# Optimization experiments

Hardware: AMD Instinct MI355X
Metric: run time of the kernel (lower is better)

Reference implementation:

```python
import jax, jax.numpy as jnp
import numpy as np

WIN = 2
PC = 48
IMG = 128
D = PC * WIN * WIN      # token dim == state dim N == 192
NS = IMG // WIN          # 64
L = NS * NS              # 4096 tokens
BATCH = 2


def setup_inputs() -> dict:
    key = jax.random.key(0)
    ks = jax.random.split(key, 8)
    s = 1.0 / np.sqrt(D)  # nn.Linear default init scale
    x = jax.random.normal(ks[0], (BATCH, PC, IMG, IMG), jnp.float32)
    A_log = jnp.log(jax.random.uniform(ks[1], (D, D), jnp.float32, 1.0, 16.0))
    D_param = jnp.ones((D,), jnp.float32)
    W_B = jax.random.uniform(ks[2], (D, D), jnp.float32, -s, s)
    b_B = jax.random.uniform(ks[3], (D,), jnp.float32, -s, s)
    W_C = jax.random.uniform(ks[4], (D, D), jnp.float32, -s, s)
    b_C = jax.random.uniform(ks[5], (D,), jnp.float32, -s, s)
    W_dt = jax.random.uniform(ks[6], (D, D), jnp.float32, -s, s)
    b_dt = jax.random.uniform(ks[7], (D,), jnp.float32, -s, s)
    return {"x": x, "A_log": A_log, "D_param": D_param, "W_B": W_B, "b_B": b_B,
            "W_C": W_C, "b_C": b_C, "W_dt": W_dt, "b_dt": b_dt}


def _forward(x, A_log, D_param, W_B, b_B, W_C, b_C, W_dt, b_dt):
    Bb, C, H, W = x.shape
    w = WIN
    # unfold into non-overlapping windows -> tokens (B, L, D) with D = C*w*w (channel-major)
    t = x.reshape(Bb, C, H // w, w, W // w, w).transpose(0, 1, 2, 4, 3, 5)
    tokens = t.reshape(Bb, C, -1, w * w).transpose(0, 2, 1, 3).reshape(Bb, -1, D)
    Bm = tokens @ W_B.T + b_B                      # (B, L, D) -> state input proj
    Cm = tokens @ W_C.T + b_C                      # (B, L, D) -> state output proj
    dt = jax.nn.softplus(tokens @ W_dt.T + b_dt)   # module applies softplus once
    # selective_scan_fn applies delta = softplus(delta + delta_bias) again (delta_softplus=True)
    delta = jax.nn.softplus(dt + b_dt)             # (B, L, D)
    A = -jnp.exp(A_log)                            # (D, N) with N == D
    u = tokens                                     # (B, L, D)

    def step(h, inp):
        d_l, u_l, B_l, C_l = inp                   # (B,D) (B,D) (B,N) (B,N)
        dA = jnp.exp(d_l[:, :, None] * A[None])    # (B, D, N)
        h = dA * h + (d_l * u_l)[:, :, None] * B_l[:, None, :]
        y = jnp.einsum('bdn,bn->bd', h, C_l)
        return h, y

    h0 = jnp.zeros((Bb, D, D), x.dtype)
    xs = (delta.transpose(1, 0, 2), u.transpose(1, 0, 2),
          Bm.transpose(1, 0, 2), Cm.transpose(1, 0, 2))
    _, ys = jax.lax.scan(step, h0, xs)             # (L, B, D)
    y = ys.transpose(1, 2, 0)                      # (B, D, L)
    y = y + D_param[None, :, None] * u.transpose(0, 2, 1)
    z = jnp.ones_like(y)                           # z = ones in the module
    y = y * (z * jax.nn.sigmoid(z))                # silu(z) gating
    out = y.reshape(Bb, NS, NS, PC, w, w).transpose(0, 3, 1, 4, 2, 5)
    return out.reshape(Bb, PC, NS * w, NS * w)


def reference(x, A_log, D_param, W_B, b_B, W_C, b_C, W_dt, b_dt):
    return _forward(x, A_log, D_param, W_B, b_B, W_C, b_C, W_dt, b_dt)
```

## Files before the change

kernel.cpp:

```cpp
#include <hip/hip_runtime.h>
#include <hip/hip_bf16.h>
#include <math.h>

#define BB   2
#define PCH  48
#define DD   192
#define NSB  64
#define LL   4096
#define NCH  128
#define LCH  32
#define WUP  12
#define NG   8
#define NCK  24
#define SILU1 0.7310585786300049f

typedef float v2f __attribute__((ext_vector_type(2)));
typedef float v4f __attribute__((ext_vector_type(4)));
typedef __bf16 bf16x8 __attribute__((ext_vector_type(8)));
typedef float f32x4 __attribute__((ext_vector_type(4)));

#if __has_builtin(__builtin_amdgcn_exp2f)
#define EXP2(x) __builtin_amdgcn_exp2f(x)
#else
#define EXP2(x) exp2f(x)
#endif

#if __has_builtin(__builtin_elementwise_fma)
static __device__ __forceinline__ v2f fma2(v2f a, v2f b, v2f c) {
    return __builtin_elementwise_fma(a, b, c);
}
#else
static __device__ __forceinline__ v2f fma2(v2f a, v2f b, v2f c) {
    v2f r; r.x = __builtin_fmaf(a.x, b.x, c.x); r.y = __builtin_fmaf(a.y, b.y, c.y);
    return r;
}
#endif

static __device__ __forceinline__ float softplus_(float x) {
    return fmaxf(x, 0.0f) + log1pf(__expf(-fabsf(x)));
}

static __device__ __forceinline__ unsigned short f2bf(float f) {
    unsigned int u = __builtin_bit_cast(unsigned int, f);
    u += 0x7fffu + ((u >> 16) & 1u);
    return (unsigned short)(u >> 16);
}

__global__ void k_tok(const float* __restrict__ x, float* __restrict__ tokens,
                      float* __restrict__ u_t,
                      const float* __restrict__ A_log, float* __restrict__ A2t,
                      const float* __restrict__ W_B, const float* __restrict__ W_C,
                      const float* __restrict__ W_dt,
                      unsigned short* __restrict__ tok_bf,
                      unsigned short* __restrict__ W_bf) {
    __shared__ float lds[64 * 196];
    int b  = blockIdx.x >> 6;
    int hb = blockIdx.x & 63;
    int tid = threadIdx.x;
    for (int t = blockIdx.x * 256 + tid; t < DD * DD; t += 128 * 256) {
        int n = t / DD, d = t - n * DD;
        A2t[t] = -__expf(A_log[d * DD + n]) * 1.4426950408889634f;
    }
    for (int t = blockIdx.x * 256 + tid; t < 3 * DD * DD; t += 128 * 256) {
        int mat = t / (DD * DD), r = t - mat * DD * DD;
        const float* W = (mat == 0) ? W_B : (mat == 1 ? W_C : W_dt);
        W_bf[t] = f2bf(W[r]);
    }
    for (int idx = tid; idx < 48 * 2 * 128; idx += 256) {
        int c = idx >> 8; int r = idx & 255; int i = r >> 7; int w = r & 127;
        float v = x[((b * 48 + c) * 128 + (hb * 2 + i)) * 128 + w];
        int wb = w >> 1, j = w & 1;
        lds[wb * 196 + c * 4 + i * 2 + j] = v;
    }
    __syncthreads();
    for (int idx = tid; idx < 64 * 192; idx += 256) {
        int wb = idx / 192, d = idx - wb * 192;
        float v = lds[wb * 196 + d];
        size_t o = (size_t)(b * 4096 + hb * 64 + wb) * 192 + d;
        tokens[o] = v;
        tok_bf[o] = f2bf(v);
    }
    for (int idx = tid; idx < 64 * 192; idx += 256) {
        int d = idx >> 6, wb = idx & 63;
        u_t[(size_t)(b * 192 + d) * 4096 + hb * 64 + wb] = lds[wb * 196 + d];
    }
}

__global__ __launch_bounds__(256) void k_proj(
        const unsigned short* __restrict__ tok_bf,
        const unsigned short* __restrict__ W_bf,
        const float* __restrict__ b_B, const float* __restrict__ b_C,
        const float* __restrict__ b_dt,
        float* __restrict__ Bm, float* __restrict__ Cm,
        float* __restrict__ delta) {
    int tid  = threadIdx.x;
    int lane = tid & 63;
    int wv   = tid >> 6;
    int m0   = blockIdx.x * 16;
    int mat  = blockIdx.y;
    int lrow = lane & 15;
    int koff = (lane >> 4) * 8;

    const unsigned short* ap = tok_bf + (size_t)(m0 + lrow) * 192 + koff;
    bf16x8 a[6];
    #pragma unroll
    for (int k0 = 0; k0 < 6; ++k0)
        a[k0] = *reinterpret_cast<const bf16x8*>(ap + k0 * 32);

    f32x4 acc[3];
    #pragma unroll
    for (int jt = 0; jt < 3; ++jt) {
        #pragma unroll
        for (int r = 0; r < 4; ++r) acc[jt][r] = 0.f;
    }
    #pragma unroll
    for (int jt = 0; jt < 3; ++jt) {
        int j = wv * 48 + jt * 16 + lrow;
        const unsigned short* bp = W_bf + (size_t)(mat * 192 + j) * 192 + koff;
        #pragma unroll
        for (int k0 = 0; k0 < 6; ++k0) {
            bf16x8 bv = *reinterpret_cast<const bf16x8*>(bp + k0 * 32);
            acc[jt] = __builtin_amdgcn_mfma_f32_16x16x32_bf16(a[k0], bv, acc[jt],
                                                              0, 0, 0);
        }
    }

    int col = lane & 15;
    int rb  = (lane >> 4) * 4;
    #pragma unroll
    for (int jt = 0; jt < 3; ++jt) {
        int j = wv * 48 + jt * 16 + col;
        #pragma unroll
        for (int r = 0; r < 4; ++r) {
            int m = m0 + rb + r;
            float z = acc[jt][r];
            size_t o = (size_t)m * 192 + j;
            if (mat == 0)       Bm[o] = z + b_B[j];
            else if (mat == 1)  Cm[o] = z + b_C[j];
            else {
                float bd = b_dt[j];
                delta[o] = softplus_(softplus_(z + bd) + bd);
            }
        }
    }
}

__global__ __launch_bounds__(512, 6) void k_scan(
        const float* __restrict__ delta, const float* __restrict__ tokens,
        const float* __restrict__ Bm, const float* __restrict__ Cm,
        const float* __restrict__ A2t, float* __restrict__ y_t) {
    __shared__ float ytile[LCH * 65];
    int tid = threadIdx.x;
    for (int i = tid; i < LCH * 65; i += 512) ytile[i] = 0.0f;
    __syncthreads();

    int lane = tid & 63;
    int ng   = tid >> 6;
    int blk  = blockIdx.x;
    int c    = blk & (NCH - 1);
    int rest = blk >> 7;
    int dg   = rest % 3, b = rest / 3;
    int d    = dg * 64 + lane;
    int n0   = ng * NCK;

    v2f A2[NCK / 2], h[NCK / 2];
    #pragma unroll
    for (int p = 0; p < NCK / 2; ++p) {
        A2[p].x = A2t[(n0 + 2 * p) * 192 + d];
        A2[p].y = A2t[(n0 + 2 * p + 1) * 192 + d];
        h[p].x = 0.f; h[p].y = 0.f;
    }

    int l0     = c * LCH;
    int nwarm  = (c == 0) ? 0 : WUP;
    int base   = (b * 4096 + l0 - nwarm) * 192;
    int ubase  = __builtin_amdgcn_readfirstlane(base + n0);
    const float* bp = Bm + ubase;
    const float* cp = Cm + ubase;
    const float* dp = delta + base + d;
    const float* up = tokens + base + d;

    float dlt = dp[0], uv = up[0];
    int s = 0;
    #pragma unroll 4
    for (int t = 0; t < nwarm; ++t, ++s) {
        float dn = dp[(s + 1) * 192], un = up[(s + 1) * 192];
        const v4f* B4 = (const v4f*)(bp + s * 192);
        v4f bq[NCK / 4];
        #pragma unroll
        for (int q = 0; q < NCK / 4; ++q) bq[q] = B4[q];
        float du = dlt * uv;
        v2f dlt2; dlt2.x = dlt; dlt2.y = dlt;
        v2f du2;  du2.x = du;   du2.y = du;
        #pragma unroll
        for (int q = 0; q < NCK / 4; ++q) {
            v2f blo = __builtin_shufflevector(bq[q], bq[q], 0, 1);
            v2f bhi = __builtin_shufflevector(bq[q], bq[q], 2, 3);
            v2f e0 = dlt2 * A2[2 * q];
            v2f e1 = dlt2 * A2[2 * q + 1];
            v2f dA0; dA0.x = EXP2(e0.x); dA0.y = EXP2(e0.y);
            v2f dA1; dA1.x = EXP2(e1.x); dA1.y = EXP2(e1.y);
            h[2 * q]     = fma2(dA0, h[2 * q],     du2 * blo);
            h[2 * q + 1] = fma2(dA1, h[2 * q + 1], du2 * bhi);
        }
        dlt = dn; uv = un;
    }
    #pragma unroll 4
    for (int t = 0; t < LCH; ++t, ++s) {
        float dn = dp[(s + 1) * 192], un = up[(s + 1) * 192];
        const v4f* B4 = (const v4f*)(bp + s * 192);
        const v4f* C4 = (const v4f*)(cp + s * 192);
        v4f bq[NCK / 4], cq[NCK / 4];
        #pragma unroll
        for (int q = 0; q < NCK / 4; ++q) { bq[q] = B4[q]; cq[q] = C4[q]; }
        float du = dlt * uv;
        v2f dlt2; dlt2.x = dlt; dlt2.y = dlt;
        v2f du2;  du2.x = du;   du2.y = du;
        v2f acc2; acc2.x = 0.f; acc2.y = 0.f;
        #pragma unroll
        for (int q = 0; q < NCK / 4; ++q) {
            v2f blo = __builtin_shufflevector(bq[q], bq[q], 0, 1);
            v2f bhi = __builtin_shufflevector(bq[q], bq[q], 2, 3);
            v2f clo = __builtin_shufflevector(cq[q], cq[q], 0, 1);
            v2f chi = __builtin_shufflevector(cq[q], cq[q], 2, 3);
            v2f e0 = dlt2 * A2[2 * q];
            v2f e1 = dlt2 * A2[2 * q + 1];
            v2f dA0; dA0.x = EXP2(e0.x); dA0.y = EXP2(e0.y);
            v2f dA1; dA1.x = EXP2(e1.x); dA1.y = EXP2(e1.y);
            h[2 * q]     = fma2(dA0, h[2 * q],     du2 * blo);
            h[2 * q + 1] = fma2(dA1, h[2 * q + 1], du2 * bhi);
            acc2 = fma2(h[2 * q],     clo, acc2);
            acc2 = fma2(h[2 * q + 1], chi, acc2);
        }
        atomicAdd(&ytile[t * 65 + lane], acc2.x + acc2.y);
        dlt = dn; uv = un;
    }
    __syncthreads();
    for (int idx = tid; idx < LCH * 64; idx += 512) {
        int dd = idx >> 5, t = idx & (LCH - 1);
        y_t[((size_t)(b * 192 + dg * 64 + dd)) * 4096 + l0 + t] =
            ytile[t * 65 + dd];
    }
}

__global__ void k_fin(const float* __restrict__ y_t, const float* __restrict__ u_t,
                      const float* __restrict__ Dp, float* __restrict__ out) {
    __shared__ float v[3 * 4224];
    int b  = blockIdx.x >> 6;
    int a1 = blockIdx.x & 63;
    int d0 = 3 * a1;
    int tid = threadIdx.x;
    for (int idx = tid; idx < 3 * 4096; idx += 256) {
        int e = idx >> 12, l = idx & 4095;
        size_t o = ((size_t)(b * 192 + d0 + e)) * 4096 + l;
        float val = (y_t[o] + Dp[d0 + e] * u_t[o]) * SILU1;
        v[e * 4224 + l + (l >> 5)] = val;
    }
    __syncthreads();
    for (int o = tid; o < 12288; o += 256) {
        int cc = o >> 8;
        int i  = (o >> 7) & 1;
        int w  = o & 127;
        int a2 = w >> 1, j = w & 1;
        int r  = a2 * 192 + cc * 4 + i * 2 + j;
        int e  = r >> 12, l = r & 4095;
        out[((size_t)((b * 48 + cc) * 128 + (a1 * 2 + i))) * 128 + w] =
            v[e * 4224 + l + (l >> 5)];
    }
}

extern "C" void kernel_launch(void* const* d_in, const int* in_sizes, int n_in,
                              void* d_out, int out_size, void* d_ws, size_t ws_size,
                              hipStream_t stream) {
    const float* x     = (const float*)d_in[0];
    const float* A_log = (const float*)d_in[1];
    const float* Dp    = (const float*)d_in[2];
    const float* W_B   = (const float*)d_in[3];
    const float* b_B   = (const float*)d_in[4];
    const float* W_C   = (const float*)d_in[5];
    const float* b_C   = (const float*)d_in[6];
    const float* W_dt  = (const float*)d_in[7];
    const float* b_dt  = (const float*)d_in[8];
    float* out = (float*)d_out;

    const size_t TOK = (size_t)BB * LL * DD;
    float* ws = (float*)d_ws;
    float* tokens = ws;
    float* u_t    = tokens + TOK;
    float* Bm     = u_t + TOK;
    float* Cm     = Bm + TOK;
    float* delta  = Cm + TOK;
    float* A2t    = delta + TOK;
    float* y_t    = A2t + (size_t)DD * DD;
    unsigned short* tok_bf = (unsigned short*)(y_t + TOK);
    unsigned short* W_bf   = tok_bf + TOK;

    k_tok<<<dim3(BB * NSB), dim3(256), 0, stream>>>(x, tokens, u_t, A_log, A2t,
                                                    W_B, W_C, W_dt, tok_bf, W_bf);
    k_proj<<<dim3(512, 3), dim3(256), 0, stream>>>(tok_bf, W_bf, b_B, b_C, b_dt,
                                                   Bm, Cm, delta);
    k_scan<<<dim3(BB * 3 * NCH), dim3(512), 0, stream>>>(delta, tokens, Bm, Cm,
                                                         A2t, y_t);
    k_fin<<<dim3(BB * NSB), dim3(256), 0, stream>>>(y_t, u_t, Dp, out);
}
```

Before: 129.6 us.

## Fuse finalize epilogue into scan kernel and drop u_t/y_t intermediates

The scan kernel now caches each chunk's u values in shared memory, applies the D skip term and the constant SiLU gate, and writes straight into the output image layout. This removes the k_fin launch, the transposed u_t store in k_tok, and the y_t round-trip through global memory. In exchange the output stores from the scan epilogue are scattered with integer div/mod index math and are poorly coalesced, and the scan uses a little more shared memory.

```diff
diff --git a/kernel.cpp b/kernel.cpp
--- a/kernel.cpp
+++ b/kernel.cpp
@@ -47,7 +47,6 @@
 }
 
 __global__ void k_tok(const float* __restrict__ x, float* __restrict__ tokens,
-                      float* __restrict__ u_t,
                       const float* __restrict__ A_log, float* __restrict__ A2t,
                       const float* __restrict__ W_B, const float* __restrict__ W_C,
                       const float* __restrict__ W_dt,
@@ -79,10 +78,6 @@
         size_t o = (size_t)(b * 4096 + hb * 64 + wb) * 192 + d;
         tokens[o] = v;
         tok_bf[o] = f2bf(v);
-    }
-    for (int idx = tid; idx < 64 * 192; idx += 256) {
-        int d = idx >> 6, wb = idx & 63;
-        u_t[(size_t)(b * 192 + d) * 4096 + hb * 64 + wb] = lds[wb * 196 + d];
     }
 }
 
@@ -148,8 +143,10 @@
 __global__ __launch_bounds__(512, 6) void k_scan(
         const float* __restrict__ delta, const float* __restrict__ tokens,
         const float* __restrict__ Bm, const float* __restrict__ Cm,
-        const float* __restrict__ A2t, float* __restrict__ y_t) {
+        const float* __restrict__ A2t, const float* __restrict__ Dp,
+        float* __restrict__ out) {
     __shared__ float ytile[LCH * 65];
+    __shared__ float utile[LCH * 65];
     int tid = threadIdx.x;
     for (int i = tid; i < LCH * 65; i += 512) ytile[i] = 0.0f;
     __syncthreads();
@@ -208,6 +205,7 @@
     #pragma unroll 4
     for (int t = 0; t < LCH; ++t, ++s) {
         float dn = dp[(s + 1) * 192], un = up[(s + 1) * 192];
+        if (ng == 0) utile[t * 65 + lane] = uv;
         const v4f* B4 = (const v4f*)(bp + s * 192);
         const v4f* C4 = (const v4f*)(cp + s * 192);
         v4f bq[NCK / 4], cq[NCK / 4];
@@ -236,36 +234,20 @@
         dlt = dn; uv = un;
     }
     __syncthreads();
+
+    #pragma unroll 1
     for (int idx = tid; idx < LCH * 64; idx += 512) {
         int dd = idx >> 5, t = idx & (LCH - 1);
-        y_t[((size_t)(b * 192 + dg * 64 + dd)) * 4096 + l0 + t] =
-            ytile[t * 65 + dd];
-    }
-}
-
-__global__ void k_fin(const float* __restrict__ y_t, const float* __restrict__ u_t,
-                      const float* __restrict__ Dp, float* __restrict__ out) {
-    __shared__ float v[3 * 4224];
-    int b  = blockIdx.x >> 6;
-    int a1 = blockIdx.x & 63;
-    int d0 = 3 * a1;
-    int tid = threadIdx.x;
-    for (int idx = tid; idx < 3 * 4096; idx += 256) {
-        int e = idx >> 12, l = idx & 4095;
-        size_t o = ((size_t)(b * 192 + d0 + e)) * 4096 + l;
-        float val = (y_t[o] + Dp[d0 + e] * u_t[o]) * SILU1;
-        v[e * 4224 + l + (l >> 5)] = val;
-    }
-    __syncthreads();
-    for (int o = tid; o < 12288; o += 256) {
-        int cc = o >> 8;
-        int i  = (o >> 7) & 1;
-        int w  = o & 127;
-        int a2 = w >> 1, j = w & 1;
-        int r  = a2 * 192 + cc * 4 + i * 2 + j;
-        int e  = r >> 12, l = r & 4095;
-        out[((size_t)((b * 48 + cc) * 128 + (a1 * 2 + i))) * 128 + w] =
-            v[e * 4224 + l + (l >> 5)];
+        int de = dg * 64 + dd;
+        int q  = de / 3, rem = de - 3 * q;
+        int l  = l0 + t;
+        int inner = rem * 4096 + l;
+        int a2 = inner / 192;
+        int m  = inner - 192 * a2;
+        int pc = m >> 2, oi = (m >> 1) & 1, oj = m & 1;
+        float val = (ytile[t * 65 + dd] + Dp[de] * utile[t * 65 + dd]) * SILU1;
+        out[((size_t)((b * 48 + pc) * 128 + 2 * q + oi)) * 128 + 2 * a2 + oj] =
+            val;
     }
 }
 
@@ -286,20 +268,17 @@
     const size_t TOK = (size_t)BB * LL * DD;
     float* ws = (float*)d_ws;
     float* tokens = ws;
-    float* u_t    = tokens + TOK;
-    float* Bm     = u_t + TOK;
+    float* Bm     = tokens + TOK;
     float* Cm     = Bm + TOK;
     float* delta  = Cm + TOK;
     float* A2t    = delta + TOK;
-    float* y_t    = A2t + (size_t)DD * DD;
-    unsigned short* tok_bf = (unsigned short*)(y_t + TOK);
+    unsigned short* tok_bf = (unsigned short*)(A2t + (size_t)DD * DD);
     unsigned short* W_bf   = tok_bf + TOK;
 
-    k_tok<<<dim3(BB * NSB), dim3(256), 0, stream>>>(x, tokens, u_t, A_log, A2t,
+    k_tok<<<dim3(BB * NSB), dim3(256), 0, stream>>>(x, tokens, A_log, A2t,
                                                     W_B, W_C, W_dt, tok_bf, W_bf);
     k_proj<<<dim3(512, 3), dim3(256), 0, stream>>>(tok_bf, W_bf, b_B, b_C, b_dt,
                                                    Bm, Cm, delta);
     k_scan<<<dim3(BB * 3 * NCH), dim3(512), 0, stream>>>(delta, tokens, Bm, Cm,
-                                                         A2t, y_t);
-    k_fin<<<dim3(BB * NSB), dim3(256), 0, stream>>>(y_t, u_t, Dp, out);
-}
+                                                         A2t, Dp, out);
+}
```

After: 121.9 us. -5.9%, faster.
